# Kernel optimization log

Measured on AMD Instinct MI355X. Metric: run time of the kernel, lower is better.

The kernel has to match this reference:

```python
import jax, jax.numpy as jnp
import numpy as np

N = 50000
E = 800000
F = 64
HID = 64
HEADS = 4
NTYPES = 3


def layer_norm(x, g, b, eps=1e-5):
    mu = x.mean(-1, keepdims=True)
    var = ((x - mu) ** 2).mean(-1, keepdims=True)
    return (x - mu) * jax.lax.rsqrt(var + eps) * g + b


def gat_conv(x, src, dst, n, W, att_src, att_dst, bias, concat):
    # PyG GATConv: per-head linear transform, additive attention, segment softmax over dst.
    H, C = att_src.shape
    xp = (x @ W).reshape(n, H, C)                       # [N,H,C]
    a_s = (xp * att_src).sum(-1)                         # [N,H]
    a_d = (xp * att_dst).sum(-1)                         # [N,H]
    e = jax.nn.leaky_relu(a_s[src] + a_d[dst], 0.2)      # [Etot,H]
    m = jax.ops.segment_max(e, dst, num_segments=n)      # stable softmax per target
    ex = jnp.exp(e - m[dst])
    denom = jax.ops.segment_sum(ex, dst, num_segments=n)
    alpha = ex / (denom[dst] + 1e-16)                    # [Etot,H]
    msg = xp[src] * alpha[:, :, None]                    # [Etot,H,C]
    out = jax.ops.segment_sum(msg, dst, num_segments=n)  # [N,H,C]
    out = out.reshape(n, H * C) if concat else out.mean(1)
    return out + bias


def setup_inputs() -> dict:
    key = jax.random.key(0)
    ks = jax.random.split(key, 12)
    f32 = jnp.float32
    return {
        'node_features': jax.random.normal(ks[0], (N, F), f32),
        'node_types': jax.random.randint(ks[1], (N,), 0, NTYPES),
        'edge_index': jax.random.randint(ks[2], (2, E), 0, N),
        'type_emb': jax.random.normal(ks[3], (NTYPES, HID), f32) * 0.02,
        'proj_W': jax.random.normal(ks[4], (F, HID), f32) / np.sqrt(F).astype(np.float32),
        'proj_b': jnp.zeros((HID,), f32),
        'W0': jax.random.normal(ks[5], (HID, HEADS * HID), f32) / np.sqrt(HID).astype(np.float32),
        'att_src0': jax.random.normal(ks[6], (HEADS, HID), f32) * 0.1,
        'att_dst0': jax.random.normal(ks[7], (HEADS, HID), f32) * 0.1,
        'bias0': jnp.zeros((HEADS * HID,), f32),
        'ln0_g': jnp.ones((HEADS * HID,), f32),
        'ln0_b': jnp.zeros((HEADS * HID,), f32),
        'W1': jax.random.normal(ks[8], (HEADS * HID, HEADS * HID), f32) / np.sqrt(HEADS * HID).astype(np.float32),
        'att_src1': jax.random.normal(ks[9], (HEADS, HID), f32) * 0.1,
        'att_dst1': jax.random.normal(ks[10], (HEADS, HID), f32) * 0.1,
        'bias1': jnp.zeros((HID,), f32),
        'ln1_g': jnp.ones((HID,), f32),
        'ln1_b': jnp.zeros((HID,), f32),
    }


def reference(node_features, node_types, edge_index, type_emb, proj_W, proj_b,
              W0, att_src0, att_dst0, bias0, ln0_g, ln0_b,
              W1, att_src1, att_dst1, bias1, ln1_g, ln1_b):
    n = node_features.shape[0]
    loop = jnp.arange(n)
    src = jnp.concatenate([edge_index[0], loop])  # add_self_loops=True (PyG default)
    dst = jnp.concatenate([edge_index[1], loop])
    # input projection + node-type embedding
    x = node_features @ proj_W + proj_b + type_emb[node_types]
    # layer 0: concat heads -> [N, HEADS*HID]
    h = gat_conv(x, src, dst, n, W0, att_src0, att_dst0, bias0, True)
    h = jax.nn.relu(layer_norm(h, ln0_g, ln0_b))  # dropout is identity in eval
    # layer 1: mean over heads -> [N, HID]; residual skipped (shape mismatch 256 vs 64)
    h2 = gat_conv(h, src, dst, n, W1, att_src1, att_dst1, bias1, False)
    h2 = jax.nn.relu(layer_norm(h2, ln1_g, ln1_b))
    return h2
```

## Files before the change

### kernel.cpp

```cpp
#include <hip/hip_runtime.h>
#include <hip/hip_bf16.h>
#include <hip/hip_fp16.h>

typedef unsigned short u16;
typedef unsigned int u32;
typedef short s16x8 __attribute__((ext_vector_type(8)));
typedef float f32x4 __attribute__((ext_vector_type(4)));

__device__ __forceinline__ float bf2f(u16 u) {
  return __uint_as_float(((u32)u) << 16);
}

__device__ __forceinline__ u16 f2b(float f) {
  __hip_bfloat16 h = __float2bfloat16(f);
  return *(u16*)&h;
}

__device__ __forceinline__ bool sniff_bf16(const void* ones) {
  u32 w = *(const u32*)ones;
  return (w >> 16) == (w & 0xFFFFu);
}

__device__ __forceinline__ float ldf(const void* p, size_t i, bool bf) {
  return bf ? bf2f(((const u16*)p)[i]) : ((const float*)p)[i];
}

__global__ void fill_f32(float* __restrict__ p, float v, size_t n) {
  size_t i = (size_t)blockIdx.x * blockDim.x + threadIdx.x;
  if (i < n) p[i] = v;
}

__global__ __launch_bounds__(256) void deg_count_k(const int* __restrict__ ei, int E, int N,
                                                   int* __restrict__ deg) {
  int i = blockIdx.x * 256 + threadIdx.x;
  if (i >= E + N) return;
  int d = (i < E) ? ei[E + i] : (i - E);
  atomicAdd(deg + d, 1);
}

__global__ __launch_bounds__(256) void scan_local_k(const int* __restrict__ deg,
                                                    int* __restrict__ off,
                                                    int* __restrict__ bsum, int N) {
  __shared__ int ps[256];
  int t = threadIdx.x;
  int i = blockIdx.x * 256 + t;
  int v = (i < N) ? deg[i] : 0;
  ps[t] = v;
  __syncthreads();
#pragma unroll
  for (int o = 1; o < 256; o <<= 1) {
    int u = (t >= o) ? ps[t - o] : 0;
    __syncthreads();
    ps[t] += u;
    __syncthreads();
  }
  if (i < N) off[i] = ps[t] - v;
  if (t == 255) bsum[blockIdx.x] = ps[255];
}

__global__ __launch_bounds__(1024) void scan_bsum_k(int* __restrict__ bsum, int nb) {
  __shared__ int ps[1024];
  int t = threadIdx.x;
  int v = (t < nb) ? bsum[t] : 0;
  ps[t] = v;
  __syncthreads();
#pragma unroll
  for (int o = 1; o < 1024; o <<= 1) {
    int u = (t >= o) ? ps[t - o] : 0;
    __syncthreads();
    ps[t] += u;
    __syncthreads();
  }
  if (t < nb) bsum[t] = ps[t] - v;
}

__global__ __launch_bounds__(256) void scan_add_k(int* __restrict__ off,
                                                  const int* __restrict__ bsum,
                                                  int* __restrict__ cur, int N, int Etot) {
  int i = blockIdx.x * 256 + threadIdx.x;
  if (i == 0) off[N] = Etot;
  if (i >= N) return;
  int o = off[i] + bsum[i >> 8];
  off[i] = o;
  cur[i] = o;
}

__global__ __launch_bounds__(256) void scatter_k(const int* __restrict__ ei, int E, int N,
                                                 int* __restrict__ cur, int* __restrict__ csr) {
  int i = blockIdx.x * 256 + threadIdx.x;
  if (i >= E + N) return;
  int s, d;
  if (i < E) { s = ei[i]; d = ei[E + i]; } else { s = i - E; d = s; }
  int p = atomicAdd(cur + d, 1);
  csr[p] = s;
}

__global__ __launch_bounds__(256) void wpack_k(const void* __restrict__ W,
                                               const void* __restrict__ ones,
                                               u16* __restrict__ Wp, int K) {
  bool bf = sniff_bf16(ones);
  int i = blockIdx.x * 256 + threadIdx.x;
  if (i >= K * 256) return;
  int j = i & 7;
  int q = (i >> 3) & 3;
  int c = (i >> 5) & 255;
  int kc = i >> 13;
  int k = kc * 32 + q * 8 + j;
  Wp[i] = f2b(ldf(W, (size_t)k * 256 + c, bf));
}

__global__ __launch_bounds__(256) void wpack64_k(const void* __restrict__ W,
                                                 const void* __restrict__ ones,
                                                 u16* __restrict__ Wp) {
  bool bf = sniff_bf16(ones);
  int i = blockIdx.x * 256 + threadIdx.x;
  if (i >= 64 * 64) return;
  int j = i & 7;
  int q = (i >> 3) & 3;
  int c = (i >> 5) & 63;
  int kc = i >> 11;
  int k = kc * 32 + q * 8 + j;
  Wp[i] = f2b(ldf(W, (size_t)k * 64 + c, bf));
}

__global__ __launch_bounds__(256) void l0_gemm_k(
    const void* __restrict__ nf, const int* __restrict__ ntype,
    const u16* __restrict__ Wpp, const void* __restrict__ pbias,
    const void* __restrict__ temb, const u16* __restrict__ Wp,
    const void* __restrict__ atts, const void* __restrict__ attd,
    const void* __restrict__ ones,
    u16* __restrict__ C, float* __restrict__ aS, float* __restrict__ aD, int N) {
  bool bf = sniff_bf16(ones);
  __shared__ u16 xs[16][64];
  int t = threadIdx.x;
  int wave = t >> 6, lane = t & 63;
  int r = lane & 15, q = lane >> 4;
  int row0 = blockIdx.x * 16;
  int arow = row0 + r;
  if (arow >= N) arow = N - 1;
  f32x4 xacc = {0.f, 0.f, 0.f, 0.f};
#pragma unroll
  for (int kc = 0; kc < 2; kc++) {
    s16x8 a;
    if (bf) {
      a = *(const s16x8*)((const u16*)nf + (size_t)arow * 64 + kc * 32 + q * 8);
    } else {
      const float* fp = (const float*)nf + (size_t)arow * 64 + kc * 32 + q * 8;
#pragma unroll
      for (int j = 0; j < 8; j++) a[j] = (short)f2b(fp[j]);
    }
    int c = wave * 16 + r;
    s16x8 b = *(const s16x8*)(Wpp + (((size_t)kc * 64 + c) * 4 + q) * 8);
    xacc = __builtin_amdgcn_mfma_f32_16x16x32_bf16(a, b, xacc, 0, 0, 0);
  }
#pragma unroll
  for (int rg = 0; rg < 4; rg++) {
    int row = row0 + q * 4 + rg;
    int rl = (row < N) ? row : N - 1;
    int col = wave * 16 + r;
    int ty = ntype[rl];
    float v = xacc[rg] + ldf(pbias, col, bf) + ldf(temb, ty * 64 + col, bf);
    xs[q * 4 + rg][col] = f2b(v);
  }
  __syncthreads();
  int colw = wave * 64;
  f32x4 acc[4] = {{0.f, 0.f, 0.f, 0.f}, {0.f, 0.f, 0.f, 0.f},
                  {0.f, 0.f, 0.f, 0.f}, {0.f, 0.f, 0.f, 0.f}};
#pragma unroll
  for (int kc = 0; kc < 2; kc++) {
    s16x8 a = *(const s16x8*)&xs[r][kc * 32 + q * 8];
#pragma unroll
    for (int ct = 0; ct < 4; ct++) {
      int c = colw + ct * 16 + r;
      s16x8 b = *(const s16x8*)(Wp + (((size_t)kc * 256 + c) * 4 + q) * 8);
      acc[ct] = __builtin_amdgcn_mfma_f32_16x16x32_bf16(a, b, acc[ct], 0, 0, 0);
    }
  }
#pragma unroll
  for (int ct = 0; ct < 4; ct++) {
#pragma unroll
    for (int rg = 0; rg < 4; rg++) {
      int row = row0 + q * 4 + rg;
      if (row < N) C[(size_t)row * 256 + colw + ct * 16 + r] = f2b(acc[ct][rg]);
    }
  }
  float sp[4] = {0.f, 0.f, 0.f, 0.f};
  float dp[4] = {0.f, 0.f, 0.f, 0.f};
#pragma unroll
  for (int ct = 0; ct < 4; ct++) {
    int c = colw + ct * 16 + r;
    float av = ldf(atts, c, bf);
    float dv = ldf(attd, c, bf);
#pragma unroll
    for (int rg = 0; rg < 4; rg++) {
      sp[rg] += acc[ct][rg] * av;
      dp[rg] += acc[ct][rg] * dv;
    }
  }
#pragma unroll
  for (int o = 1; o < 16; o <<= 1) {
#pragma unroll
    for (int rg = 0; rg < 4; rg++) {
      sp[rg] += __shfl_xor(sp[rg], o, 64);
      dp[rg] += __shfl_xor(dp[rg], o, 64);
    }
  }
  if (r == 0) {
#pragma unroll
    for (int rg = 0; rg < 4; rg++) {
      int row = row0 + q * 4 + rg;
      if (row < N) {
        aS[(size_t)row * 4 + wave] = sp[rg];
        aD[(size_t)row * 4 + wave] = dp[rg];
      }
    }
  }
}

template <int K>
__global__ __launch_bounds__(256) void gemm_mfma_k(
    const u16* __restrict__ A, const u16* __restrict__ Wp,
    const void* __restrict__ atts, const void* __restrict__ attd,
    const void* __restrict__ ones,
    u16* __restrict__ C, float* __restrict__ aS, float* __restrict__ aD, int N) {
  bool bf = sniff_bf16(ones);
  int t = threadIdx.x;
  int wave = t >> 6, lane = t & 63;
  int r = lane & 15, q = lane >> 4;
  int row0 = blockIdx.x * 16;
  int colw = wave * 64;
  int arow = row0 + r;
  if (arow >= N) arow = N - 1;
  const u16* ap = A + (size_t)arow * K + q * 8;
  f32x4 acc[4] = {{0.f, 0.f, 0.f, 0.f}, {0.f, 0.f, 0.f, 0.f},
                  {0.f, 0.f, 0.f, 0.f}, {0.f, 0.f, 0.f, 0.f}};
#pragma unroll
  for (int kc = 0; kc < K / 32; kc++) {
    s16x8 a = *(const s16x8*)(ap + kc * 32);
#pragma unroll
    for (int ct = 0; ct < 4; ct++) {
      int c = colw + ct * 16 + r;
      s16x8 b = *(const s16x8*)(Wp + (((size_t)kc * 256 + c) * 4 + q) * 8);
      acc[ct] = __builtin_amdgcn_mfma_f32_16x16x32_bf16(a, b, acc[ct], 0, 0, 0);
    }
  }
#pragma unroll
  for (int ct = 0; ct < 4; ct++) {
#pragma unroll
    for (int rg = 0; rg < 4; rg++) {
      int row = row0 + q * 4 + rg;
      if (row < N) C[(size_t)row * 256 + colw + ct * 16 + r] = f2b(acc[ct][rg]);
    }
  }
  float sp[4] = {0.f, 0.f, 0.f, 0.f};
  float dp[4] = {0.f, 0.f, 0.f, 0.f};
#pragma unroll
  for (int ct = 0; ct < 4; ct++) {
    int c = colw + ct * 16 + r;
    float av = ldf(atts, c, bf);
    float dv = ldf(attd, c, bf);
#pragma unroll
    for (int rg = 0; rg < 4; rg++) {
      sp[rg] += acc[ct][rg] * av;
      dp[rg] += acc[ct][rg] * dv;
    }
  }
#pragma unroll
  for (int o = 1; o < 16; o <<= 1) {
#pragma unroll
    for (int rg = 0; rg < 4; rg++) {
      sp[rg] += __shfl_xor(sp[rg], o, 64);
      dp[rg] += __shfl_xor(dp[rg], o, 64);
    }
  }
  if (r == 0) {
#pragma unroll
    for (int rg = 0; rg < 4; rg++) {
      int row = row0 + q * 4 + rg;
      if (row < N) {
        aS[(size_t)row * 4 + wave] = sp[rg];
        aD[(size_t)row * 4 + wave] = dp[rg];
      }
    }
  }
}

template <int LAYER>
__global__ __launch_bounds__(256) void agg_fused_k(
    const int* __restrict__ off, const int* __restrict__ csr,
    const float* __restrict__ aS, const float* __restrict__ aD,
    const u16* __restrict__ xp,
    const void* __restrict__ bias, const void* __restrict__ g,
    const void* __restrict__ b, void* __restrict__ out, int N) {
  bool bf = sniff_bf16(g);
  int n = blockIdx.x * 4 + (threadIdx.x >> 6);
  int lane = threadIdx.x & 63;
  if (n >= N) return;
  int start = off[n], end = off[n + 1];
  float4 ad4 = *(const float4*)(aD + (size_t)n * 4);
  float ad[4] = {ad4.x, ad4.y, ad4.z, ad4.w};
  float den[4] = {0.f, 0.f, 0.f, 0.f};
  float acc[4] = {0.f, 0.f, 0.f, 0.f};

  for (int cs = start; cs < end; cs += 64) {
    int cnt = end - cs; if (cnt > 64) cnt = 64;
    int s = 0;
    int w01 = 0, w23 = 0;
    if (lane < cnt) {
      s = csr[cs + lane];
      float4 as4 = *(const float4*)(aS + (size_t)s * 4);
      float av[4] = {as4.x, as4.y, as4.z, as4.w};
      float ex[4];
#pragma unroll
      for (int h = 0; h < 4; h++) {
        float v = av[h] + ad[h];
        v = (v > 0.f ? v : 0.2f * v) - 3.0f;
        ex[h] = __expf(v);
        den[h] += ex[h];
      }
      __half2 p01 = __floats2half2_rn(ex[0], ex[1]);
      __half2 p23 = __floats2half2_rn(ex[2], ex[3]);
      w01 = *(int*)&p01;
      w23 = *(int*)&p23;
    }
#pragma unroll 4
    for (int e = 0; e < cnt; e++) {
      int se = __shfl(s, e, 64);
      int u01 = __shfl(w01, e, 64);
      int u23 = __shfl(w23, e, 64);
      __half2 h01 = *(__half2*)&u01;
      __half2 h23 = *(__half2*)&u23;
      float w0 = __low2float(h01), w1 = __high2float(h01);
      float w2 = __low2float(h23), w3 = __high2float(h23);
      const u16* xr = xp + (size_t)se * 256;
      acc[0] += w0 * bf2f(xr[lane]);
      acc[1] += w1 * bf2f(xr[64 + lane]);
      acc[2] += w2 * bf2f(xr[128 + lane]);
      acc[3] += w3 * bf2f(xr[192 + lane]);
    }
  }
#pragma unroll
  for (int h = 0; h < 4; h++) {
#pragma unroll
    for (int o = 32; o > 0; o >>= 1) den[h] += __shfl_xor(den[h], o, 64);
    acc[h] /= (den[h] + 1e-16f);
  }

  if (LAYER == 0) {
    float y[4];
    float sum = 0.f;
#pragma unroll
    for (int h = 0; h < 4; h++) {
      y[h] = acc[h] + ldf(bias, h * 64 + lane, bf);
      sum += y[h];
    }
#pragma unroll
    for (int o = 32; o > 0; o >>= 1) sum += __shfl_xor(sum, o, 64);
    float mu = sum * (1.f / 256.f);
    float sq = 0.f;
#pragma unroll
    for (int h = 0; h < 4; h++) { float dv = y[h] - mu; sq += dv * dv; }
#pragma unroll
    for (int o = 32; o > 0; o >>= 1) sq += __shfl_xor(sq, o, 64);
    float inv = rsqrtf(sq * (1.f / 256.f) + 1e-5f);
#pragma unroll
    for (int h = 0; h < 4; h++) {
      int c = h * 64 + lane;
      float o_ = (y[h] - mu) * inv * ldf(g, c, bf) + ldf(b, c, bf);
      ((u16*)out)[(size_t)n * 256 + c] = f2b(fmaxf(o_, 0.f));
    }
  } else {
    float z = 0.25f * (acc[0] + acc[1] + acc[2] + acc[3]) + ldf(bias, lane, bf);
    float sum = z;
#pragma unroll
    for (int o = 32; o > 0; o >>= 1) sum += __shfl_xor(sum, o, 64);
    float mu = sum * (1.f / 64.f);
    float dv = z - mu;
    float sq = dv * dv;
#pragma unroll
    for (int o = 32; o > 0; o >>= 1) sq += __shfl_xor(sq, o, 64);
    float y = dv * rsqrtf(sq * (1.f / 64.f) + 1e-5f) * ldf(g, lane, bf) + ldf(b, lane, bf);
    y = fmaxf(y, 0.f);
    if (bf) ((__hip_bfloat16*)out)[(size_t)n * 64 + lane] = __float2bfloat16(y);
    else    ((float*)out)[(size_t)n * 64 + lane] = y;
  }
}

extern "C" void kernel_launch(void* const* d_in, const int* in_sizes, int n_in,
                              void* d_out, int out_size, void* d_ws, size_t ws_size,
                              hipStream_t stream) {
  const void* nf   = d_in[0];
  const int* ntyp  = (const int*)d_in[1];
  const int* ei    = (const int*)d_in[2];
  const void* temb = d_in[3];
  const void* pW   = d_in[4];
  const void* pb   = d_in[5];
  const void* W0   = d_in[6];
  const void* as0  = d_in[7];
  const void* ad0  = d_in[8];
  const void* b0   = d_in[9];
  const void* g0   = d_in[10];
  const void* be0  = d_in[11];
  const void* W1   = d_in[12];
  const void* as1  = d_in[13];
  const void* ad1  = d_in[14];
  const void* b1   = d_in[15];
  const void* g1   = d_in[16];
  const void* be1  = d_in[17];

  int N = in_sizes[0] / 64;
  int E = in_sizes[2] / 2;
  int Etot = E + N;

  u16* Wp0 = (u16*)d_ws;
  u16* Wp1 = Wp0 + 64 * 256;
  u16* Wpp = Wp1 + 256 * 256;
  u16* A   = Wpp + 64 * 64;
  u16* hb  = A + (size_t)N * 256;
  float* aS = (float*)(hb + (size_t)N * 256);
  float* aD = aS + (size_t)N * 4;
  int* deg  = (int*)(aD + (size_t)N * 4);
  int* off  = deg + N;
  int* csr  = off + N + 1;
  int* bsum = csr + Etot;

  dim3 b256(256);
  int nodeBlocks = (N + 3) / 4;
  int edgeBlocksT = (Etot + 255) / 256;
  int gemmBlocks = (N + 15) / 16;
  int scanBlocks = (N + 255) / 256;

  fill_f32<<<(N + 255) / 256, b256, 0, stream>>>((float*)deg, 0.f, (size_t)N);
  deg_count_k<<<edgeBlocksT, b256, 0, stream>>>(ei, E, N, deg);
  scan_local_k<<<scanBlocks, b256, 0, stream>>>(deg, off, bsum, N);
  scan_bsum_k<<<1, 1024, 0, stream>>>(bsum, scanBlocks);
  scan_add_k<<<scanBlocks, b256, 0, stream>>>(off, bsum, deg, N, Etot);
  scatter_k<<<edgeBlocksT, b256, 0, stream>>>(ei, E, N, deg, csr);
  wpack_k<<<(64 * 256 + 255) / 256, b256, 0, stream>>>(W0, g0, Wp0, 64);
  wpack_k<<<(256 * 256 + 255) / 256, b256, 0, stream>>>(W1, g0, Wp1, 256);
  wpack64_k<<<(64 * 64 + 255) / 256, b256, 0, stream>>>(pW, g0, Wpp);

  l0_gemm_k<<<gemmBlocks, b256, 0, stream>>>(nf, ntyp, Wpp, pb, temb, Wp0, as0, ad0, g0,
                                             A, aS, aD, N);
  agg_fused_k<0><<<nodeBlocks, b256, 0, stream>>>(off, csr, aS, aD, A, b0, g0, be0, hb, N);

  gemm_mfma_k<256><<<gemmBlocks, b256, 0, stream>>>(hb, Wp1, as1, ad1, g0, A, aS, aD, N);
  agg_fused_k<1><<<nodeBlocks, b256, 0, stream>>>(off, csr, aS, aD, A, b1, g1, be1, d_out, N);
}
```

Baseline: 429.6 us.

## Gather packed bf16 pairs per lane and broadcast edge weights via readlane

The aggregation kernel now assigns each lane two adjacent channels, so it reads one 32-bit word holding two bf16 values instead of separate 16-bit loads. This halves the gather load instructions per neighbor. Edge index and softmax weights are now broadcast with readlane using the uniform loop counter, replacing LDS-based shuffles, and the weights stay in fp32 instead of packed half. The epilogues for both layers are rewritten for the new channel mapping, including a cross-half shuffle for the head mean, and use packed bf16 stores.

```diff
diff --git a/kernel.cpp b/kernel.cpp
--- a/kernel.cpp
+++ b/kernel.cpp
@@ -16,6 +16,10 @@
   return *(u16*)&h;
 }
 
+__device__ __forceinline__ u32 packbf(float lo, float hi) {
+  return (u32)f2b(lo) | ((u32)f2b(hi) << 16);
+}
+
 __device__ __forceinline__ bool sniff_bf16(const void* ones) {
   u32 w = *(const u32*)ones;
   return (w >> 16) == (w & 0xFFFFu);
@@ -23,6 +27,10 @@
 
 __device__ __forceinline__ float ldf(const void* p, size_t i, bool bf) {
   return bf ? bf2f(((const u16*)p)[i]) : ((const float*)p)[i];
+}
+
+__device__ __forceinline__ float rdlane_f(float v, int e) {
+  return __uint_as_float((u32)__builtin_amdgcn_readlane((int)__float_as_uint(v), e));
 }
 
 __global__ void fill_f32(float* __restrict__ p, float v, size_t n) {
@@ -297,20 +305,21 @@
   int lane = threadIdx.x & 63;
   if (n >= N) return;
   int start = off[n], end = off[n + 1];
+  bool hiSel = (lane & 32) != 0;
   float4 ad4 = *(const float4*)(aD + (size_t)n * 4);
   float ad[4] = {ad4.x, ad4.y, ad4.z, ad4.w};
   float den[4] = {0.f, 0.f, 0.f, 0.f};
   float acc[4] = {0.f, 0.f, 0.f, 0.f};
+  const u32* xp32 = (const u32*)xp;
 
   for (int cs = start; cs < end; cs += 64) {
     int cnt = end - cs; if (cnt > 64) cnt = 64;
     int s = 0;
-    int w01 = 0, w23 = 0;
+    float ex[4] = {0.f, 0.f, 0.f, 0.f};
     if (lane < cnt) {
       s = csr[cs + lane];
       float4 as4 = *(const float4*)(aS + (size_t)s * 4);
       float av[4] = {as4.x, as4.y, as4.z, as4.w};
-      float ex[4];
 #pragma unroll
       for (int h = 0; h < 4; h++) {
         float v = av[h] + ad[h];
@@ -318,71 +327,87 @@
         ex[h] = __expf(v);
         den[h] += ex[h];
       }
-      __half2 p01 = __floats2half2_rn(ex[0], ex[1]);
-      __half2 p23 = __floats2half2_rn(ex[2], ex[3]);
-      w01 = *(int*)&p01;
-      w23 = *(int*)&p23;
     }
 #pragma unroll 4
     for (int e = 0; e < cnt; e++) {
-      int se = __shfl(s, e, 64);
-      int u01 = __shfl(w01, e, 64);
-      int u23 = __shfl(w23, e, 64);
-      __half2 h01 = *(__half2*)&u01;
-      __half2 h23 = *(__half2*)&u23;
-      float w0 = __low2float(h01), w1 = __high2float(h01);
-      float w2 = __low2float(h23), w3 = __high2float(h23);
-      const u16* xr = xp + (size_t)se * 256;
-      acc[0] += w0 * bf2f(xr[lane]);
-      acc[1] += w1 * bf2f(xr[64 + lane]);
-      acc[2] += w2 * bf2f(xr[128 + lane]);
-      acc[3] += w3 * bf2f(xr[192 + lane]);
+      int se = __builtin_amdgcn_readlane(s, e);
+      float w0 = rdlane_f(ex[0], e);
+      float w1 = rdlane_f(ex[1], e);
+      float w2 = rdlane_f(ex[2], e);
+      float w3 = rdlane_f(ex[3], e);
+      float wA = hiSel ? w1 : w0;
+      float wB = hiSel ? w3 : w2;
+      const u32* xr = xp32 + (size_t)se * 128 + lane;
+      u32 dA = xr[0];
+      u32 dB = xr[64];
+      acc[0] += wA * __uint_as_float(dA << 16);
+      acc[1] += wA * __uint_as_float(dA & 0xffff0000u);
+      acc[2] += wB * __uint_as_float(dB << 16);
+      acc[3] += wB * __uint_as_float(dB & 0xffff0000u);
     }
   }
 #pragma unroll
   for (int h = 0; h < 4; h++) {
 #pragma unroll
     for (int o = 32; o > 0; o >>= 1) den[h] += __shfl_xor(den[h], o, 64);
-    acc[h] /= (den[h] + 1e-16f);
+  }
+  {
+    float dA = (hiSel ? den[1] : den[0]) + 1e-16f;
+    float dB = (hiSel ? den[3] : den[2]) + 1e-16f;
+    acc[0] /= dA; acc[1] /= dA;
+    acc[2] /= dB; acc[3] /= dB;
   }
 
   if (LAYER == 0) {
+    int c0 = 2 * lane, c2 = 128 + 2 * lane;
     float y[4];
-    float sum = 0.f;
-#pragma unroll
-    for (int h = 0; h < 4; h++) {
-      y[h] = acc[h] + ldf(bias, h * 64 + lane, bf);
-      sum += y[h];
-    }
+    y[0] = acc[0] + ldf(bias, c0, bf);
+    y[1] = acc[1] + ldf(bias, c0 + 1, bf);
+    y[2] = acc[2] + ldf(bias, c2, bf);
+    y[3] = acc[3] + ldf(bias, c2 + 1, bf);
+    float sum = y[0] + y[1] + y[2] + y[3];
 #pragma unroll
     for (int o = 32; o > 0; o >>= 1) sum += __shfl_xor(sum, o, 64);
     float mu = sum * (1.f / 256.f);
     float sq = 0.f;
 #pragma unroll
-    for (int h = 0; h < 4; h++) { float dv = y[h] - mu; sq += dv * dv; }
+    for (int j = 0; j < 4; j++) { float dv = y[j] - mu; sq += dv * dv; }
 #pragma unroll
     for (int o = 32; o > 0; o >>= 1) sq += __shfl_xor(sq, o, 64);
     float inv = rsqrtf(sq * (1.f / 256.f) + 1e-5f);
-#pragma unroll
-    for (int h = 0; h < 4; h++) {
-      int c = h * 64 + lane;
-      float o_ = (y[h] - mu) * inv * ldf(g, c, bf) + ldf(b, c, bf);
-      ((u16*)out)[(size_t)n * 256 + c] = f2b(fmaxf(o_, 0.f));
-    }
+    float o0 = fmaxf((y[0] - mu) * inv * ldf(g, c0, bf) + ldf(b, c0, bf), 0.f);
+    float o1 = fmaxf((y[1] - mu) * inv * ldf(g, c0 + 1, bf) + ldf(b, c0 + 1, bf), 0.f);
+    float o2 = fmaxf((y[2] - mu) * inv * ldf(g, c2, bf) + ldf(b, c2, bf), 0.f);
+    float o3 = fmaxf((y[3] - mu) * inv * ldf(g, c2 + 1, bf) + ldf(b, c2 + 1, bf), 0.f);
+    u32* orow = (u32*)out + (size_t)n * 128;
+    orow[lane] = packbf(o0, o1);
+    orow[64 + lane] = packbf(o2, o3);
   } else {
-    float z = 0.25f * (acc[0] + acc[1] + acc[2] + acc[3]) + ldf(bias, lane, bf);
-    float sum = z;
+    float p0 = acc[0] + acc[2];
+    float p1 = acc[1] + acc[3];
+    p0 += __shfl_xor(p0, 32, 64);
+    p1 += __shfl_xor(p1, 32, 64);
+    int c = 2 * (lane & 31);
+    float z0 = 0.25f * p0 + ldf(bias, c, bf);
+    float z1 = 0.25f * p1 + ldf(bias, c + 1, bf);
+    float sum = z0 + z1;
 #pragma unroll
     for (int o = 32; o > 0; o >>= 1) sum += __shfl_xor(sum, o, 64);
-    float mu = sum * (1.f / 64.f);
-    float dv = z - mu;
-    float sq = dv * dv;
+    float mu = sum * (1.f / 128.f);
+    float d0 = z0 - mu, d1 = z1 - mu;
+    float sq = d0 * d0 + d1 * d1;
 #pragma unroll
     for (int o = 32; o > 0; o >>= 1) sq += __shfl_xor(sq, o, 64);
-    float y = dv * rsqrtf(sq * (1.f / 64.f) + 1e-5f) * ldf(g, lane, bf) + ldf(b, lane, bf);
-    y = fmaxf(y, 0.f);
-    if (bf) ((__hip_bfloat16*)out)[(size_t)n * 64 + lane] = __float2bfloat16(y);
-    else    ((float*)out)[(size_t)n * 64 + lane] = y;
+    float inv = rsqrtf(sq * (1.f / 128.f) + 1e-5f);
+    float y0 = fmaxf(d0 * inv * ldf(g, c, bf) + ldf(b, c, bf), 0.f);
+    float y1 = fmaxf(d1 * inv * ldf(g, c + 1, bf) + ldf(b, c + 1, bf), 0.f);
+    if (lane < 32) {
+      if (bf) {
+        ((u32*)out)[(size_t)n * 32 + lane] = packbf(y0, y1);
+      } else {
+        ((float2*)out)[(size_t)n * 32 + lane] = make_float2(y0, y1);
+      }
+    }
   }
 }
 
```

Result: faster. 417.8 us (-2.7%).
